# Kernel optimization log

Hardware: AMD Instinct MI355X
Metric: run time of the kernel (lower is better)

Reference implementation:

```python
import jax, jax.numpy as jnp
import numpy as np

ALPHA = 0.2  # LeakyReLU negative slope
NEG_INF = -9e15


def setup_inputs() -> dict:
    key = jax.random.key(0)
    k1, k2, k3, k4 = jax.random.split(key, 4)
    B, N, Fin, Fout = 8, 2048, 512, 256
    x = jax.random.normal(k1, (B, N, Fin), dtype=jnp.float32)
    adj = jax.random.randint(k2, (B, N, N), 0, 2, dtype=jnp.int32)
    # xavier_uniform-like init, gain=1.414
    limW = 1.414 * np.sqrt(6.0 / (Fin + Fout))
    W = jax.random.uniform(k3, (Fin, Fout), jnp.float32, -limW, limW)
    lima = 1.414 * np.sqrt(6.0 / (2 * Fout + 1))
    a = jax.random.uniform(k4, (2 * Fout, 1), jnp.float32, -lima, lima)
    return {"x": x, "adj": adj, "W": W, "a": a}


def reference(x, adj, W, a):
    # x: [B,N,Fin], adj: [B,N,N], W: [Fin,Fout], a: [2*Fout,1]
    Fout = W.shape[1]
    h = jnp.einsum('bnf,fo->bno', x, W)                      # [B,N,Fout]
    a1 = a[:Fout, 0]                                         # source part
    a2 = a[Fout:, 0]                                         # target part
    # e_ij = LeakyReLU(a1.h_i + a2.h_j) -- decomposed, no O(N^2*2F) tensor
    s = h @ a1                                               # [B,N]
    t = h @ a2                                               # [B,N]
    e = jax.nn.leaky_relu(s[:, :, None] + t[:, None, :], ALPHA)  # [B,N,N]
    e = jnp.where(adj > 0, e, NEG_INF)
    attention = jax.nn.softmax(e, axis=2)                    # dropout p=0 (eval)
    h_prime = jnp.einsum('bij,bjo->bio', attention, h)       # [B,N,Fout]
    return jax.nn.elu(h_prime)                               # concat=True -> ELU
```

## Files before the change

kernel.cpp:

```cpp
#include <hip/hip_runtime.h>
#include <hip/hip_bf16.h>

typedef __attribute__((ext_vector_type(8))) short short8;
typedef __attribute__((ext_vector_type(4))) short short4v;
typedef __attribute__((ext_vector_type(4))) float f32x4;

constexpr int Bb = 8, NN = 2048, FIN = 512, FOUT = 256;
#define LRALPHA 0.2f
#define MFMA16(a, b, c) __builtin_amdgcn_mfma_f32_16x16x32_bf16((a), (b), (c), 0, 0, 0)

__device__ __forceinline__ ushort f2bf(float f) {
    unsigned u = __float_as_uint(f);
    u += 0x7fffu + ((u >> 16) & 1u);
    return (ushort)(u >> 16);
}
__device__ __forceinline__ float bf2f(ushort b) { return __uint_as_float(((unsigned)b) << 16); }

__global__ __launch_bounds__(256) void prep_w(const float* __restrict__ W,
                                              ushort* __restrict__ WTh,
                                              ushort* __restrict__ WTl) {
    const int n = blockIdx.x, t = threadIdx.x;
    for (int k = t; k < FIN; k += 256) {
        const float w = W[(size_t)k * FOUT + n];
        const ushort hi = f2bf(w);
        WTh[(size_t)n * FIN + k] = hi;
        WTl[(size_t)n * FIN + k] = f2bf(w - bf2f(hi));
    }
}

__global__ __launch_bounds__(512, 4) void gemm_h(const float* __restrict__ x,
                                                 const ushort* __restrict__ WTh,
                                                 const ushort* __restrict__ WTl,
                                                 const float* __restrict__ a,
                                                 ushort* __restrict__ hTh,
                                                 float* __restrict__ sv,
                                                 float* __restrict__ tv) {
    __shared__ ushort Ah[4][2][512];
    __shared__ ushort Tr[8][16][72];

    const int t = threadIdx.x, lane = t & 63, w = t >> 6;
    const int m0 = (blockIdx.x >> 1) * 64;
    const int n0 = (blockIdx.x & 1) * 128;

    const int ql = t & 63, qks = (t >> 6) & 1, qif = t >> 7;
    const float* xp = x + (size_t)(m0 + qif * 16 + (ql & 15)) * FIN + qks * 32 + (ql >> 4) * 8;

    const size_t boff = (size_t)(n0 + w * 16 + (lane & 15)) * FIN + (lane >> 4) * 8;
    const ushort* bph = WTh + boff;
    const ushort* bpl = WTl + boff;

    f32x4 acc[4];
#pragma unroll
    for (int f = 0; f < 4; ++f) acc[f] = (f32x4){0.f, 0.f, 0.f, 0.f};

    for (int kt = 0; kt < 8; ++kt) {
        const int k0 = kt * 64;
        const short8 bh0 = *(const short8*)(bph + k0);
        const short8 bl0 = *(const short8*)(bpl + k0);
        const short8 bh1 = *(const short8*)(bph + k0 + 32);
        const short8 bl1 = *(const short8*)(bpl + k0 + 32);
        const float4 f0 = *(const float4*)(xp + k0);
        const float4 f1 = *(const float4*)(xp + k0 + 4);
        const float fv[8] = {f0.x, f0.y, f0.z, f0.w, f1.x, f1.y, f1.z, f1.w};
        short8 vh;
#pragma unroll
        for (int e = 0; e < 8; ++e) vh[e] = (short)f2bf(fv[e]);
        __syncthreads();
        *(short8*)&Ah[qif][qks][ql * 8] = vh;
        __syncthreads();
#pragma unroll
        for (int f = 0; f < 4; ++f) {
            const short8 a0 = *(const short8*)&Ah[f][0][lane * 8];
            const short8 a1 = *(const short8*)&Ah[f][1][lane * 8];
            acc[f] = MFMA16(a0, bh0, acc[f]);
            acc[f] = MFMA16(a0, bl0, acc[f]);
            acc[f] = MFMA16(a1, bh1, acc[f]);
            acc[f] = MFMA16(a1, bl1, acc[f]);
        }
    }

    const int cc = n0 + w * 16 + (lane & 15);
    const float a1v = a[cc], a2v = a[FOUT + cc];
    const int rb = (lane >> 4) * 4;
#pragma unroll
    for (int f = 0; f < 4; ++f) {
#pragma unroll
        for (int r = 0; r < 4; ++r) {
            float v1 = acc[f][r] * a1v;
            float v2 = acc[f][r] * a2v;
#pragma unroll
            for (int m = 1; m < 16; m <<= 1) {
                v1 += __shfl_xor(v1, m, 16);
                v2 += __shfl_xor(v2, m, 16);
            }
            if ((lane & 15) == 0) {
                atomicAdd(&sv[m0 + f * 16 + rb + r], v1);
                atomicAdd(&tv[m0 + f * 16 + rb + r], v2);
            }
        }
    }

#pragma unroll
    for (int f = 0; f < 4; ++f)
#pragma unroll
        for (int r = 0; r < 4; ++r)
            Tr[w][lane & 15][f * 16 + rb + r] = f2bf(acc[f][r]);
    __syncthreads();
    const int c = lane >> 2, rowb = (lane & 3) * 16;
    const ushort* src = &Tr[w][c][rowb];
    const short8 v0 = *(const short8*)src;
    const short8 v1 = *(const short8*)(src + 8);
    ushort* dst = hTh + ((size_t)(m0 >> 11) * FOUT + n0 + w * 16 + c) * NN + (m0 & 2047) + rowb;
    *(short8*)dst = v0;
    *(short8*)(dst + 8) = v1;
}

__global__ __launch_bounds__(512, 4) void gat_fused(const int* __restrict__ adj,
                                                    const ushort* __restrict__ hTh,
                                                    const float* __restrict__ sv,
                                                    const float* __restrict__ tv,
                                                    float* __restrict__ out) {
    __shared__ float t_l[NN];
    __shared__ ushort Pf[2][2][2][512];
    __shared__ float den_sl[32][17];
    __shared__ float den_l[32];

    const int t = threadIdx.x, lane = t & 63, w = t >> 6;
    const int b = blockIdx.x & 7, i0 = (blockIdx.x >> 3) * 32;

    *(float4*)&t_l[t * 4] = *(const float4*)&tv[b * NN + t * 4];

    const int pf_ = t >> 8, pks = (t >> 7) & 1, pl = (t >> 1) & 63, ph = t & 1;
    const int prow = (pf_ << 4) | (pl & 15);
    const int pj = (pks << 5) | ((pl >> 4) << 3) | (ph << 2);
    const int slot = ph | ((pl >> 4) << 1) | (pks << 3);
    const float s_i = sv[b * NN + i0 + prow];
    const int* adjp = adj + ((size_t)b * NN + i0 + prow) * NN + pj;
    ushort* pdst0 = &Pf[0][pf_][pks][pl * 8 + ph * 4];
    ushort* pdst1 = &Pf[1][pf_][pks][pl * 8 + ph * 4];

    const ushort* hb = hTh + (size_t)b * FOUT * NN;
    const ushort* h00 = hb + (size_t)(2 * w * 16 + (lane & 15)) * NN + (lane >> 4) * 8;
    const ushort* h10 = hb + (size_t)((2 * w + 1) * 16 + (lane & 15)) * NN + (lane >> 4) * 8;

    f32x4 acc[2][2];
#pragma unroll
    for (int f = 0; f < 2; ++f)
#pragma unroll
        for (int cf = 0; cf < 2; ++cf) acc[f][cf] = (f32x4){0.f, 0.f, 0.f, 0.f};
    float den_part = 0.f;

    int4 ajv = *(const int4*)adjp;
    short8 X00 = *(const short8*)h00, X01 = *(const short8*)(h00 + 32);
    short8 X10 = *(const short8*)h10, X11 = *(const short8*)(h10 + 32);
    short8 Y00, Y01, Y10, Y11;

    __syncthreads();

    auto phase = [&](int jt, int rbuf, ushort* pdst,
                     short8& c00, short8& c01, short8& c10, short8& c11,
                     short8& n00, short8& n01, short8& n10, short8& n11) {
        const int j0 = jt * 64;
        const int jn = min(j0 + 64, NN - 64);
        const int4 ajn = *(const int4*)(adjp + jn);
        n00 = *(const short8*)(h00 + jn);
        n01 = *(const short8*)(h00 + jn + 32);
        n10 = *(const short8*)(h10 + jn);
        n11 = *(const short8*)(h10 + jn + 32);
        const float4 tq = *(const float4*)&t_l[j0 + pj];
        const float tvv[4] = {tq.x, tq.y, tq.z, tq.w};
        const int avs[4] = {ajv.x, ajv.y, ajv.z, ajv.w};
        short4v pv;
#pragma unroll
        for (int e = 0; e < 4; ++e) {
            float v = s_i + tvv[e];
            v = v > 0.f ? v : LRALPHA * v;
            const float wv = avs[e] > 0 ? __expf(v) : 0.f;
            const ushort hbv = f2bf(wv);
            den_part += bf2f(hbv);
            pv[e] = (short)hbv;
        }
        *(short4v*)pdst = pv;
        ajv = ajn;
        __syncthreads();
        const short8 a00 = *(const short8*)&Pf[rbuf][0][0][lane * 8];
        const short8 a01 = *(const short8*)&Pf[rbuf][0][1][lane * 8];
        const short8 a10 = *(const short8*)&Pf[rbuf][1][0][lane * 8];
        const short8 a11 = *(const short8*)&Pf[rbuf][1][1][lane * 8];
        __builtin_amdgcn_s_setprio(1);
        acc[0][0] = MFMA16(a00, c00, acc[0][0]);
        acc[0][0] = MFMA16(a01, c01, acc[0][0]);
        acc[0][1] = MFMA16(a00, c10, acc[0][1]);
        acc[0][1] = MFMA16(a01, c11, acc[0][1]);
        acc[1][0] = MFMA16(a10, c00, acc[1][0]);
        acc[1][0] = MFMA16(a11, c01, acc[1][0]);
        acc[1][1] = MFMA16(a10, c10, acc[1][1]);
        acc[1][1] = MFMA16(a11, c11, acc[1][1]);
        __builtin_amdgcn_s_setprio(0);
    };

    for (int tt = 0; tt < NN / 64; tt += 2) {
        phase(tt, 0, pdst0, X00, X01, X10, X11, Y00, Y01, Y10, Y11);
        phase(tt + 1, 1, pdst1, Y00, Y01, Y10, Y11, X00, X01, X10, X11);
    }

    den_sl[prow][slot] = den_part;
    __syncthreads();
    if (t < 32) {
        float s = 0.f;
#pragma unroll
        for (int k = 0; k < 16; ++k) s += den_sl[t][k];
        den_l[t] = s;
    }
    __syncthreads();

    const int rb = (lane >> 4) * 4;
#pragma unroll
    for (int f = 0; f < 2; ++f) {
#pragma unroll
        for (int r = 0; r < 4; ++r) {
            const int row = f * 16 + rb + r;
            const float inv = 1.0f / den_l[row];
#pragma unroll
            for (int cf = 0; cf < 2; ++cf) {
                float v = acc[f][cf][r] * inv;
                v = v > 0.f ? v : expm1f(v);
                out[((size_t)b * NN + i0 + row) * FOUT + w * 32 + cf * 16 + (lane & 15)] = v;
            }
        }
    }
}

extern "C" void kernel_launch(void* const* d_in, const int* in_sizes, int n_in,
                              void* d_out, int out_size, void* d_ws, size_t ws_size,
                              hipStream_t stream) {
    const float* x   = (const float*)d_in[0];
    const int*   adj = (const int*)d_in[1];
    const float* W   = (const float*)d_in[2];
    const float* a   = (const float*)d_in[3];
    float* out = (float*)d_out;

    ushort* hTh = (ushort*)d_ws;
    float*  sv  = (float*)(hTh + (size_t)Bb * FOUT * NN);
    float*  tv  = sv + Bb * NN;
    ushort* WTh = (ushort*)(tv + Bb * NN);
    ushort* WTl = WTh + (size_t)FIN * FOUT;

    hipMemsetAsync(sv, 0, 2 * (size_t)Bb * NN * sizeof(float), stream);
    prep_w<<<256, 256, 0, stream>>>(W, WTh, WTl);
    gemm_h<<<512, 512, 0, stream>>>(x, WTh, WTl, a, hTh, sv, tv);
    gat_fused<<<512, 512, 0, stream>>>(adj, hTh, sv, tv, out);
}
```

Baseline: 298.5 us.

## Precompute W·a vectors, drop atomics and memset, deepen prefetch pipelines

The prep kernel now also computes W·a1 and W·a2, so gemm_h can form s and t as dot products of x with those vectors. This replaces the per-tile shuffle reductions and global atomicAdds, and removes the memset of sv/tv. gemm_h gains register double-buffering of the x and W loads, with x prefetched two tiles ahead and barriers reduced to raw s_barrier plus lgkmcnt waits. gat_fused prefetches adjacency two tiles ahead. The s/t values now come from fp32 x·(W·a) instead of the bf16 split-product h, which changes rounding slightly, and the deeper prefetch raises register pressure.

```diff
diff --git a/kernel.cpp b/kernel.cpp
--- a/kernel.cpp
+++ b/kernel.cpp
@@ -9,33 +9,58 @@
 #define LRALPHA 0.2f
 #define MFMA16(a, b, c) __builtin_amdgcn_mfma_f32_16x16x32_bf16((a), (b), (c), 0, 0, 0)
 
-__device__ __forceinline__ ushort f2bf(float f) {
+static __device__ __forceinline__ ushort f2bf(float f) {
     unsigned u = __float_as_uint(f);
     u += 0x7fffu + ((u >> 16) & 1u);
     return (ushort)(u >> 16);
 }
-__device__ __forceinline__ float bf2f(ushort b) { return __uint_as_float(((unsigned)b) << 16); }
-
-__global__ __launch_bounds__(256) void prep_w(const float* __restrict__ W,
-                                              ushort* __restrict__ WTh,
-                                              ushort* __restrict__ WTl) {
-    const int n = blockIdx.x, t = threadIdx.x;
-    for (int k = t; k < FIN; k += 256) {
-        const float w = W[(size_t)k * FOUT + n];
-        const ushort hi = f2bf(w);
-        WTh[(size_t)n * FIN + k] = hi;
-        WTl[(size_t)n * FIN + k] = f2bf(w - bf2f(hi));
+static __device__ __forceinline__ float bf2f(ushort b) { return __uint_as_float(((unsigned)b) << 16); }
+
+#define LDSBAR() do { asm volatile("s_waitcnt lgkmcnt(0)" ::: "memory"); \
+                      __builtin_amdgcn_s_barrier(); \
+                      asm volatile("" ::: "memory"); } while (0)
+#define BARONLY() do { asm volatile("" ::: "memory"); \
+                       __builtin_amdgcn_s_barrier(); \
+                       asm volatile("" ::: "memory"); } while (0)
+
+__global__ __launch_bounds__(256) void prep(const float* __restrict__ W,
+                                            const float* __restrict__ a,
+                                            ushort* __restrict__ WTh,
+                                            ushort* __restrict__ WTl,
+                                            float* __restrict__ wa1,
+                                            float* __restrict__ wa2) {
+    __shared__ float r1[4], r2[4];
+    const int k = blockIdx.x, n = threadIdx.x;
+    const int lane = n & 63, wv = n >> 6;
+    const float w = W[(size_t)k * FOUT + n];
+    const ushort hi = f2bf(w);
+    WTh[(size_t)n * FIN + k] = hi;
+    WTl[(size_t)n * FIN + k] = f2bf(w - bf2f(hi));
+    float p1 = w * a[n], p2 = w * a[FOUT + n];
+#pragma unroll
+    for (int m = 1; m < 64; m <<= 1) {
+        p1 += __shfl_xor(p1, m);
+        p2 += __shfl_xor(p2, m);
+    }
+    if (lane == 0) { r1[wv] = p1; r2[wv] = p2; }
+    __syncthreads();
+    if (n == 0) {
+        wa1[k] = r1[0] + r1[1] + r1[2] + r1[3];
+        wa2[k] = r2[0] + r2[1] + r2[2] + r2[3];
     }
 }
 
 __global__ __launch_bounds__(512, 4) void gemm_h(const float* __restrict__ x,
                                                  const ushort* __restrict__ WTh,
                                                  const ushort* __restrict__ WTl,
-                                                 const float* __restrict__ a,
+                                                 const float* __restrict__ wa1,
+                                                 const float* __restrict__ wa2,
                                                  ushort* __restrict__ hTh,
                                                  float* __restrict__ sv,
                                                  float* __restrict__ tv) {
     __shared__ ushort Ah[4][2][512];
+    __shared__ float SR1[64][8];
+    __shared__ float SR2[64][8];
     __shared__ ushort Tr[8][16][72];
 
     const int t = threadIdx.x, lane = t & 63, w = t >> 6;
@@ -43,7 +68,9 @@
     const int n0 = (blockIdx.x & 1) * 128;
 
     const int ql = t & 63, qks = (t >> 6) & 1, qif = t >> 7;
-    const float* xp = x + (size_t)(m0 + qif * 16 + (ql & 15)) * FIN + qks * 32 + (ql >> 4) * 8;
+    const int kcol = qks * 32 + (ql >> 4) * 8;
+    const int arow = qif * 16 + (ql & 15);
+    const float* xp = x + (size_t)(m0 + arow) * FIN + kcol;
 
     const size_t boff = (size_t)(n0 + w * 16 + (lane & 15)) * FIN + (lane >> 4) * 8;
     const ushort* bph = WTh + boff;
@@ -52,60 +79,77 @@
     f32x4 acc[4];
 #pragma unroll
     for (int f = 0; f < 4; ++f) acc[f] = (f32x4){0.f, 0.f, 0.f, 0.f};
-
-    for (int kt = 0; kt < 8; ++kt) {
+    float sp = 0.f, tp = 0.f;
+
+    float4 xa0 = *(const float4*)(xp + 0),  xa1 = *(const float4*)(xp + 4);
+    float4 xb0 = *(const float4*)(xp + 64), xb1 = *(const float4*)(xp + 68);
+    float4 xc0, xc1, xd0, xd1;
+    short8 bhA0 = *(const short8*)(bph + 0),  blA0 = *(const short8*)(bpl + 0);
+    short8 bhA1 = *(const short8*)(bph + 32), blA1 = *(const short8*)(bpl + 32);
+    short8 bhB0, blB0, bhB1, blB1;
+
+    auto phase = [&](int kt, const float4& c0, const float4& c1, float4& n0_, float4& n1_,
+                     const short8& cbh0, const short8& cbl0, const short8& cbh1, const short8& cbl1,
+                     short8& nbh0, short8& nbl0, short8& nbh1, short8& nbl1) {
         const int k0 = kt * 64;
-        const short8 bh0 = *(const short8*)(bph + k0);
-        const short8 bl0 = *(const short8*)(bpl + k0);
-        const short8 bh1 = *(const short8*)(bph + k0 + 32);
-        const short8 bl1 = *(const short8*)(bpl + k0 + 32);
-        const float4 f0 = *(const float4*)(xp + k0);
-        const float4 f1 = *(const float4*)(xp + k0 + 4);
-        const float fv[8] = {f0.x, f0.y, f0.z, f0.w, f1.x, f1.y, f1.z, f1.w};
+        const float fv[8] = {c0.x, c0.y, c0.z, c0.w, c1.x, c1.y, c1.z, c1.w};
         short8 vh;
 #pragma unroll
         for (int e = 0; e < 8; ++e) vh[e] = (short)f2bf(fv[e]);
-        __syncthreads();
+        const float4 w1a = *(const float4*)(wa1 + k0 + kcol);
+        const float4 w1b = *(const float4*)(wa1 + k0 + kcol + 4);
+        const float4 w2a = *(const float4*)(wa2 + k0 + kcol);
+        const float4 w2b = *(const float4*)(wa2 + k0 + kcol + 4);
+        sp += fv[0]*w1a.x + fv[1]*w1a.y + fv[2]*w1a.z + fv[3]*w1a.w
+            + fv[4]*w1b.x + fv[5]*w1b.y + fv[6]*w1b.z + fv[7]*w1b.w;
+        tp += fv[0]*w2a.x + fv[1]*w2a.y + fv[2]*w2a.z + fv[3]*w2a.w
+            + fv[4]*w2b.x + fv[5]*w2b.y + fv[6]*w2b.z + fv[7]*w2b.w;
+        BARONLY();
         *(short8*)&Ah[qif][qks][ql * 8] = vh;
-        __syncthreads();
+        LDSBAR();
+        const int kx = (kt + 2 < 8 ? kt + 2 : 7) * 64;
+        n0_ = *(const float4*)(xp + kx);
+        n1_ = *(const float4*)(xp + kx + 4);
+        const int kb = (kt + 1 < 8 ? kt + 1 : 7) * 64;
+        nbh0 = *(const short8*)(bph + kb);
+        nbl0 = *(const short8*)(bpl + kb);
+        nbh1 = *(const short8*)(bph + kb + 32);
+        nbl1 = *(const short8*)(bpl + kb + 32);
 #pragma unroll
         for (int f = 0; f < 4; ++f) {
             const short8 a0 = *(const short8*)&Ah[f][0][lane * 8];
             const short8 a1 = *(const short8*)&Ah[f][1][lane * 8];
-            acc[f] = MFMA16(a0, bh0, acc[f]);
-            acc[f] = MFMA16(a0, bl0, acc[f]);
-            acc[f] = MFMA16(a1, bh1, acc[f]);
-            acc[f] = MFMA16(a1, bl1, acc[f]);
+            acc[f] = MFMA16(a0, cbh0, acc[f]);
+            acc[f] = MFMA16(a0, cbl0, acc[f]);
+            acc[f] = MFMA16(a1, cbh1, acc[f]);
+            acc[f] = MFMA16(a1, cbl1, acc[f]);
         }
-    }
-
-    const int cc = n0 + w * 16 + (lane & 15);
-    const float a1v = a[cc], a2v = a[FOUT + cc];
+    };
+
+    for (int kt = 0; kt < 8; kt += 4) {
+        phase(kt + 0, xa0, xa1, xc0, xc1, bhA0, blA0, bhA1, blA1, bhB0, blB0, bhB1, blB1);
+        phase(kt + 1, xb0, xb1, xd0, xd1, bhB0, blB0, bhB1, blB1, bhA0, blA0, bhA1, blA1);
+        phase(kt + 2, xc0, xc1, xa0, xa1, bhA0, blA0, bhA1, blA1, bhB0, blB0, bhB1, blB1);
+        phase(kt + 3, xd0, xd1, xb0, xb1, bhB0, blB0, bhB1, blB1, bhA0, blA0, bhA1, blA1);
+    }
+
+    SR1[arow][qks * 4 + (ql >> 4)] = sp;
+    SR2[arow][qks * 4 + (ql >> 4)] = tp;
+
     const int rb = (lane >> 4) * 4;
-#pragma unroll
-    for (int f = 0; f < 4; ++f) {
-#pragma unroll
-        for (int r = 0; r < 4; ++r) {
-            float v1 = acc[f][r] * a1v;
-            float v2 = acc[f][r] * a2v;
-#pragma unroll
-            for (int m = 1; m < 16; m <<= 1) {
-                v1 += __shfl_xor(v1, m, 16);
-                v2 += __shfl_xor(v2, m, 16);
-            }
-            if ((lane & 15) == 0) {
-                atomicAdd(&sv[m0 + f * 16 + rb + r], v1);
-                atomicAdd(&tv[m0 + f * 16 + rb + r], v2);
-            }
-        }
-    }
-
 #pragma unroll
     for (int f = 0; f < 4; ++f)
 #pragma unroll
         for (int r = 0; r < 4; ++r)
             Tr[w][lane & 15][f * 16 + rb + r] = f2bf(acc[f][r]);
     __syncthreads();
+    if (t < 64 && n0 == 0) {
+        float s = 0.f, tt2 = 0.f;
+#pragma unroll
+        for (int q = 0; q < 8; ++q) { s += SR1[t][q]; tt2 += SR2[t][q]; }
+        sv[m0 + t] = s;
+        tv[m0 + t] = tt2;
+    }
     const int c = lane >> 2, rowb = (lane & 3) * 16;
     const ushort* src = &Tr[w][c][rowb];
     const short8 v0 = *(const short8*)src;
@@ -143,33 +187,33 @@
     const ushort* h00 = hb + (size_t)(2 * w * 16 + (lane & 15)) * NN + (lane >> 4) * 8;
     const ushort* h10 = hb + (size_t)((2 * w + 1) * 16 + (lane & 15)) * NN + (lane >> 4) * 8;
 
-    f32x4 acc[2][2];
-#pragma unroll
-    for (int f = 0; f < 2; ++f)
-#pragma unroll
-        for (int cf = 0; cf < 2; ++cf) acc[f][cf] = (f32x4){0.f, 0.f, 0.f, 0.f};
+    f32x4 acc00 = {0.f,0.f,0.f,0.f}, acc01 = acc00, acc10 = acc00, acc11 = acc00;
     float den_part = 0.f;
 
-    int4 ajv = *(const int4*)adjp;
+    int4 ajA = *(const int4*)(adjp);
+    int4 ajB = *(const int4*)(adjp + 64);
+    int4 ajC, ajD;
     short8 X00 = *(const short8*)h00, X01 = *(const short8*)(h00 + 32);
     short8 X10 = *(const short8*)h10, X11 = *(const short8*)(h10 + 32);
     short8 Y00, Y01, Y10, Y11;
 
     __syncthreads();
 
-    auto phase = [&](int jt, int rbuf, ushort* pdst,
-                     short8& c00, short8& c01, short8& c10, short8& c11,
+    auto phase = [&](int jt, ushort* pdst, int rbuf,
+                     const int4& ajcur, int4& aj2,
+                     const short8& c00, const short8& c01, const short8& c10, const short8& c11,
                      short8& n00, short8& n01, short8& n10, short8& n11) {
         const int j0 = jt * 64;
-        const int jn = min(j0 + 64, NN - 64);
-        const int4 ajn = *(const int4*)(adjp + jn);
-        n00 = *(const short8*)(h00 + jn);
-        n01 = *(const short8*)(h00 + jn + 32);
-        n10 = *(const short8*)(h10 + jn);
-        n11 = *(const short8*)(h10 + jn + 32);
+        const int jH = min(j0 + 64, NN - 64);
+        const int jA = min(j0 + 128, NN - 64);
+        n00 = *(const short8*)(h00 + jH);
+        n01 = *(const short8*)(h00 + jH + 32);
+        n10 = *(const short8*)(h10 + jH);
+        n11 = *(const short8*)(h10 + jH + 32);
+        aj2 = *(const int4*)(adjp + jA);
         const float4 tq = *(const float4*)&t_l[j0 + pj];
         const float tvv[4] = {tq.x, tq.y, tq.z, tq.w};
-        const int avs[4] = {ajv.x, ajv.y, ajv.z, ajv.w};
+        const int avs[4] = {ajcur.x, ajcur.y, ajcur.z, ajcur.w};
         short4v pv;
 #pragma unroll
         for (int e = 0; e < 4; ++e) {
@@ -181,27 +225,29 @@
             pv[e] = (short)hbv;
         }
         *(short4v*)pdst = pv;
-        ajv = ajn;
-        __syncthreads();
-        const short8 a00 = *(const short8*)&Pf[rbuf][0][0][lane * 8];
-        const short8 a01 = *(const short8*)&Pf[rbuf][0][1][lane * 8];
-        const short8 a10 = *(const short8*)&Pf[rbuf][1][0][lane * 8];
-        const short8 a11 = *(const short8*)&Pf[rbuf][1][1][lane * 8];
+        LDSBAR();
+        const ushort* pr = &Pf[rbuf][0][0][0] + lane * 8;
+        const short8 a00 = *(const short8*)(pr);
+        const short8 a01 = *(const short8*)(pr + 512);
+        const short8 a10 = *(const short8*)(pr + 1024);
+        const short8 a11 = *(const short8*)(pr + 1536);
         __builtin_amdgcn_s_setprio(1);
-        acc[0][0] = MFMA16(a00, c00, acc[0][0]);
-        acc[0][0] = MFMA16(a01, c01, acc[0][0]);
-        acc[0][1] = MFMA16(a00, c10, acc[0][1]);
-        acc[0][1] = MFMA16(a01, c11, acc[0][1]);
-        acc[1][0] = MFMA16(a10, c00, acc[1][0]);
-        acc[1][0] = MFMA16(a11, c01, acc[1][0]);
-        acc[1][1] = MFMA16(a10, c10, acc[1][1]);
-        acc[1][1] = MFMA16(a11, c11, acc[1][1]);
+        acc00 = MFMA16(a00, c00, acc00);
+        acc00 = MFMA16(a01, c01, acc00);
+        acc01 = MFMA16(a00, c10, acc01);
+        acc01 = MFMA16(a01, c11, acc01);
+        acc10 = MFMA16(a10, c00, acc10);
+        acc10 = MFMA16(a11, c01, acc10);
+        acc11 = MFMA16(a10, c10, acc11);
+        acc11 = MFMA16(a11, c11, acc11);
         __builtin_amdgcn_s_setprio(0);
     };
 
-    for (int tt = 0; tt < NN / 64; tt += 2) {
-        phase(tt, 0, pdst0, X00, X01, X10, X11, Y00, Y01, Y10, Y11);
-        phase(tt + 1, 1, pdst1, Y00, Y01, Y10, Y11, X00, X01, X10, X11);
+    for (int tt = 0; tt < NN / 64; tt += 4) {
+        phase(tt + 0, pdst0, 0, ajA, ajC, X00, X01, X10, X11, Y00, Y01, Y10, Y11);
+        phase(tt + 1, pdst1, 1, ajB, ajD, Y00, Y01, Y10, Y11, X00, X01, X10, X11);
+        phase(tt + 2, pdst0, 0, ajC, ajA, X00, X01, X10, X11, Y00, Y01, Y10, Y11);
+        phase(tt + 3, pdst1, 1, ajD, ajB, Y00, Y01, Y10, Y11, X00, X01, X10, X11);
     }
 
     den_sl[prow][slot] = den_part;
@@ -215,6 +261,7 @@
     __syncthreads();
 
     const int rb = (lane >> 4) * 4;
+    const f32x4 av[2][2] = {{acc00, acc01}, {acc10, acc11}};
 #pragma unroll
     for (int f = 0; f < 2; ++f) {
 #pragma unroll
@@ -223,7 +270,7 @@
             const float inv = 1.0f / den_l[row];
 #pragma unroll
             for (int cf = 0; cf < 2; ++cf) {
-                float v = acc[f][cf][r] * inv;
+                float v = av[f][cf][r] * inv;
                 v = v > 0.f ? v : expm1f(v);
                 out[((size_t)b * NN + i0 + row) * FOUT + w * 32 + cf * 16 + (lane & 15)] = v;
             }
@@ -245,9 +292,10 @@
     float*  tv  = sv + Bb * NN;
     ushort* WTh = (ushort*)(tv + Bb * NN);
     ushort* WTl = WTh + (size_t)FIN * FOUT;
-
-    hipMemsetAsync(sv, 0, 2 * (size_t)Bb * NN * sizeof(float), stream);
-    prep_w<<<256, 256, 0, stream>>>(W, WTh, WTl);
-    gemm_h<<<512, 512, 0, stream>>>(x, WTh, WTl, a, hTh, sv, tv);
+    float*  wa1 = (float*)(WTl + (size_t)FIN * FOUT);
+    float*  wa2 = wa1 + FIN;
+
+    prep<<<FIN, 256, 0, stream>>>(W, a, WTh, WTl, wa1, wa2);
+    gemm_h<<<512, 512, 0, stream>>>(x, WTh, WTl, wa1, wa2, hTh, sv, tv);
     gat_fused<<<512, 512, 0, stream>>>(adj, hTh, sv, tv, out);
 }
```

Result: no change. 301.9 us (+1.2%).
